# Kernel optimization log

Hardware: AMD Instinct MI355X
Metric: run time of the kernel (lower is better)

The kernel has to match this reference:

```python
import jax, jax.numpy as jnp
import numpy as np

SIZE = (128, 160, 128)  # (D, H, W)
BATCH, CHANNELS = 4, 1


def setup_inputs() -> dict:
    key = jax.random.key(0)
    k1, k2 = jax.random.split(key)
    src = jax.random.normal(k1, (BATCH, CHANNELS) + SIZE, dtype=jnp.float32)
    # near-identity affine [B, 3, 4] so most sampled coords land in-volume
    eye = jnp.concatenate([jnp.eye(3, dtype=jnp.float32), jnp.zeros((3, 1), jnp.float32)], axis=1)
    affine_matrix = eye[None] + 0.05 * jax.random.normal(k2, (BATCH, 3, 4), dtype=jnp.float32)
    return {"src": src, "affine_matrix": affine_matrix}


def _mesh_matrix(D, H, W):
    # rows: dim0 (D), dim1 (H), dim2 (W), ones  -> [4, N]
    gz, gy, gx = jnp.meshgrid(jnp.arange(D), jnp.arange(H), jnp.arange(W), indexing='ij')
    N = D * H * W
    return jnp.stack([gz.reshape(N), gy.reshape(N), gx.reshape(N),
                      jnp.ones((N,), jnp.int32)], axis=0).astype(jnp.float32)


def _trilinear_border(src, ix, iy, iz):
    # src: [B, C, D, H, W]; ix/iy/iz: [B, N] unnormalized pixel coords (x->W, y->H, z->D)
    B, C, D, H, W = src.shape
    # border padding: clamp coordinate before interpolation (matches PyTorch)
    ix = jnp.clip(ix, 0.0, W - 1.0)
    iy = jnp.clip(iy, 0.0, H - 1.0)
    iz = jnp.clip(iz, 0.0, D - 1.0)
    x0f, y0f, z0f = jnp.floor(ix), jnp.floor(iy), jnp.floor(iz)
    wx = (ix - x0f)[:, None, :]  # [B,1,N]
    wy = (iy - y0f)[:, None, :]
    wz = (iz - z0f)[:, None, :]
    x0 = x0f.astype(jnp.int32); x1 = jnp.minimum(x0 + 1, W - 1)
    y0 = y0f.astype(jnp.int32); y1 = jnp.minimum(y0 + 1, H - 1)
    z0 = z0f.astype(jnp.int32); z1 = jnp.minimum(z0 + 1, D - 1)
    flat = src.reshape(B, C, D * H * W)
    N = ix.shape[-1]

    def gather(zz, yy, xx):
        idx = (zz * H + yy) * W + xx  # [B, N]
        idx = jnp.broadcast_to(idx[:, None, :], (B, C, N))
        return jnp.take_along_axis(flat, idx, axis=2)  # [B, C, N]

    c000 = gather(z0, y0, x0); c001 = gather(z0, y0, x1)
    c010 = gather(z0, y1, x0); c011 = gather(z0, y1, x1)
    c100 = gather(z1, y0, x0); c101 = gather(z1, y0, x1)
    c110 = gather(z1, y1, x0); c111 = gather(z1, y1, x1)
    c00 = c000 + (c001 - c000) * wx
    c01 = c010 + (c011 - c010) * wx
    c10 = c100 + (c101 - c100) * wx
    c11 = c110 + (c111 - c110) * wx
    c0 = c00 + (c01 - c00) * wy
    c1 = c10 + (c11 - c10) * wy
    return c0 + (c1 - c0) * wz  # [B, C, N]


def reference(src, affine_matrix):
    D, H, W = SIZE
    B, C = src.shape[:2]
    mesh = _mesh_matrix(D, H, W)  # [4, N]
    loc = jnp.einsum('bij,jn->bin', affine_matrix, mesh)  # [B, 3, N] voxel coords
    sizes = jnp.array([D, H, W], jnp.float32)
    g = 2.0 * (loc / (sizes[None, :, None] - 1.0) - 0.5)  # normalized, dims (d0,d1,d2)
    # flip to grid_sample (x, y, z) ordering, then unnormalize (align_corners=False)
    ix = ((g[:, 2] + 1.0) * W - 1.0) * 0.5
    iy = ((g[:, 1] + 1.0) * H - 1.0) * 0.5
    iz = ((g[:, 0] + 1.0) * D - 1.0) * 0.5
    out = _trilinear_border(src, ix, iy, iz)  # [B, C, N]
    return out.reshape(B, C, D, H, W)
```

## Files before the change

kernel.cpp:

```cpp
#include <hip/hip_runtime.h>

#define DD 128
#define HH 160
#define WW 128
#define BB 4
#define HW  20480
#define DHW 2621440

#define TX 32
#define TY 8
#define TZ 8
#define XT 4
#define YT 20
#define ZT 16
#define NWG (XT * YT * ZT * BB)
#define NXCD 8
#define CPX (NWG / NXCD)

#define FZE   14
#define FYE   14
#define PITCH 44
#define CPRCH 11
#define SLABF (FYE * PITCH)
#define ROWB  (PITCH * 4)
#define SLABB (SLABF * 4)
#define SLABCH (FYE * CPRCH)
#define LDSALLOC 9216

typedef float f2 __attribute__((ext_vector_type(2), aligned(4)));
typedef float v2 __attribute__((ext_vector_type(2)));

__global__ __launch_bounds__(256)
void st_affine_kernel(const float* __restrict__ src,
                      const float* __restrict__ aff,
                      float* __restrict__ out) {
    __shared__ float lds[LDSALLOC];

    const int wgid = blockIdx.x;
    const int lin  = (wgid & (NXCD - 1)) * CPX + (wgid >> 3);
    const int xt = lin & 3;
    const int l2 = lin >> 2;
    const int yt = l2 % YT;
    const int l3 = l2 / YT;
    const int zt = l3 & (ZT - 1);
    const int b  = l3 >> 4;
    const int x0t = xt * TX, y0t = yt * TY, z0t = zt * TZ;

    const float* A = aff + b * 12;
    const float cD = 128.f/127.f, cH = 160.f/159.f, cW = 128.f/127.f;
    const float pz0 = A[0]*cD, pz1 = A[1]*cD, pz2 = A[2]*cD,  pz3 = fmaf(A[3],  cD, -0.5f);
    const float py0 = A[4]*cH, py1 = A[5]*cH, py2 = A[6]*cH,  py3 = fmaf(A[7],  cH, -0.5f);
    const float px0 = A[8]*cW, px1 = A[9]*cW, px2 = A[10]*cW, px3 = fmaf(A[11], cW, -0.5f);

    const float hz = (TZ - 1) * 0.5f, hy = (TY - 1) * 0.5f, hx = (TX - 1) * 0.5f;
    const float ccz = (float)z0t + hz, ccy = (float)y0t + hy, ccx = (float)x0t + hx;
    const float izcn = fmaf(pz0, ccz, fmaf(pz1, ccy, fmaf(pz2, ccx, pz3)));
    const float iycn = fmaf(py0, ccz, fmaf(py1, ccy, fmaf(py2, ccx, py3)));
    const float ixcn = fmaf(px0, ccz, fmaf(px1, ccy, fmaf(px2, ccx, px3)));
    const float rz = fmaf(fabsf(pz0), hz, fmaf(fabsf(pz1), hy, fmaf(fabsf(pz2), hx, 1e-3f)));
    const float ry = fmaf(fabsf(py0), hz, fmaf(fabsf(py1), hy, fmaf(fabsf(py2), hx, 1e-3f)));
    const float rx = fmaf(fabsf(px0), hz, fmaf(fabsf(px1), hy, fmaf(fabsf(px2), hx, 1e-3f)));
    const float mnz = izcn - rz, mxz = izcn + rz;
    const float mny = iycn - ry, mxy = iycn + ry;
    const float mnx = ixcn - rx, mxx = ixcn + rx;

    const bool interior =
        (mnz > 0.02f) && (mxz < 126.98f) &&
        (mny > 0.02f) && (mxy < 158.98f) &&
        (mnx > 0.02f) && (mxx < 126.98f);

    const int xlo = max(0, (int)floorf(__builtin_amdgcn_fmed3f(mnx, 0.f, 127.f)) - 1);
    const int ylo = max(0, (int)floorf(__builtin_amdgcn_fmed3f(mny, 0.f, 159.f)) - 1);
    const int zlo = max(0, (int)floorf(__builtin_amdgcn_fmed3f(mnz, 0.f, 127.f)) - 1);
    const int xhi = min(WW - 2, (int)floorf(__builtin_amdgcn_fmed3f(mxx, 0.f, 127.f)) + 1);
    const int yhi = min(HH - 2, (int)floorf(__builtin_amdgcn_fmed3f(mxy, 0.f, 159.f)) + 1);
    const int zhi = min(DD - 2, (int)floorf(__builtin_amdgcn_fmed3f(mxz, 0.f, 127.f)) + 1);

    const int xlo4 = xlo & ~3;
    const int XE4  = xhi - xlo4 + 2;
    const int YE   = yhi - ylo + 2;
    const int ZE   = zhi - zlo + 2;
    const bool fits = (XE4 <= PITCH) && (YE <= FYE) && (ZE <= FZE);

    const int tid  = threadIdx.x;
    const int lane = tid & 63;
    const int wid  = tid >> 6;

    const float zloF = (float)zlo, yloF = (float)ylo, xlo4F = (float)xlo4;

    const int xp = x0t + ((lane & 15) << 1);
    const int yo = y0t + (lane >> 4) + ((wid & 1) << 2);
    const int zb = z0t + ((wid >> 1) << 2);
    const float fx0 = (float)xp, fy = (float)yo, fzb = (float)zb;

    const float izb0 = fmaf(pz0, fzb, fmaf(pz1, fy, fmaf(pz2, fx0, pz3)));
    const float iyb0 = fmaf(py0, fzb, fmaf(py1, fy, fmaf(py2, fx0, py3)));
    const float ixb0 = fmaf(px0, fzb, fmaf(px1, fy, fmaf(px2, fx0, px3)));

    const float* sb = src + b * DHW;
    float* dst0 = out + (size_t)(((b * DD + zb) * HH + yo) * WW + xp);

    if (fits) {
        const float RC154 = 1.f / 154.f, RC11 = 1.f / 11.f;
        const float gbase = fmaf(zloF, 20480.f, fmaf(yloF, 128.f, xlo4F));
        const int totalCh = ZE * SLABCH;
        const int nIt = (totalCh + 255) >> 8;
        for (int it = 0; it < nIt; ++it) {
            const int k = (it << 8) + tid;
            float kf  = (float)k;
            float zif = floorf(fmaf(kf, RC154, 0.5f * RC154));
            float rem = fmaf(zif, -154.f, kf);
            float yif = floorf(fmaf(rem, RC11, 0.5f * RC11));
            float xif = fmaf(yif, -11.f, rem);
            float gf  = fmaf(zif, 20480.f, fmaf(yif, 128.f, fmaf(xif, 4.f, gbase)));
            int g = min((int)gf, DHW - 4);
            __builtin_amdgcn_global_load_lds(
                (const __attribute__((address_space(1))) void*)(sb + g),
                (__attribute__((address_space(3))) void*)(lds + (size_t)(((it << 8) + (wid << 6)) * 4)),
                16, 0, 0);
        }
    }
    __syncthreads();

    const char* Lb = (const char*)lds;

    auto triL = [&](int o0, int o1, v2 wx, v2 wy, v2 wz) -> v2 {
        f2 a00 = *(const f2*)(Lb + o0);
        f2 a01 = *(const f2*)(Lb + o0 + ROWB);
        f2 a10 = *(const f2*)(Lb + o0 + SLABB);
        f2 a11 = *(const f2*)(Lb + o0 + SLABB + ROWB);
        f2 b00 = *(const f2*)(Lb + o1);
        f2 b01 = *(const f2*)(Lb + o1 + ROWB);
        f2 b10 = *(const f2*)(Lb + o1 + SLABB);
        f2 b11 = *(const f2*)(Lb + o1 + SLABB + ROWB);
        v2 c00 = {fmaf(a00.y - a00.x, wx.x, a00.x), fmaf(b00.y - b00.x, wx.y, b00.x)};
        v2 c01 = {fmaf(a01.y - a01.x, wx.x, a01.x), fmaf(b01.y - b01.x, wx.y, b01.x)};
        v2 c10 = {fmaf(a10.y - a10.x, wx.x, a10.x), fmaf(b10.y - b10.x, wx.y, b10.x)};
        v2 c11 = {fmaf(a11.y - a11.x, wx.x, a11.x), fmaf(b11.y - b11.x, wx.y, b11.x)};
        v2 c0 = c00 + (c01 - c00) * wy;
        v2 c1 = c10 + (c11 - c10) * wy;
        return c0 + (c1 - c0) * wz;
    };

    if (fits) {
        const v2 dzv = {pz0, pz0}, dyv = {py0, py0}, dxv = {px0, px0};
        if (interior) {
            v2 az = {izb0 - zloF, izb0 + pz2 - zloF};
            v2 ay = {iyb0 - yloF, iyb0 + py2 - yloF};
            v2 ax = {ixb0 - xlo4F, ixb0 + px2 - xlo4F};
#pragma unroll
            for (int s = 0; s < 4; ++s) {
                v2 cz = {floorf(az.x), floorf(az.y)};
                v2 cy = {floorf(ay.x), floorf(ay.y)};
                v2 cx = {floorf(ax.x), floorf(ax.y)};
                v2 wz = az - cz, wy = ay - cy, wx = ax - cx;
                v2 ob = (cz * (float)FYE + cy) * (float)ROWB + cx * 4.f;
                v2 r = triL((int)ob.x, (int)ob.y, wx, wy, wz);
                __builtin_nontemporal_store(r, (v2*)(dst0 + s * HW));
                az += dzv; ay += dyv; ax += dxv;
            }
        } else {
            const float hiZ = 127.f - zloF, capZ = 126.f - zloF;
            const float hiY = 159.f - yloF, capY = 158.f - yloF;
            const float hiX = 127.f - xlo4F, capX = 126.f - xlo4F;
            v2 az = {izb0 - zloF, izb0 + pz2 - zloF};
            v2 ay = {iyb0 - yloF, iyb0 + py2 - yloF};
            v2 ax = {ixb0 - xlo4F, ixb0 + px2 - xlo4F};
#pragma unroll
            for (int s = 0; s < 4; ++s) {
                v2 azc = {__builtin_amdgcn_fmed3f(az.x, 0.f, hiZ),
                          __builtin_amdgcn_fmed3f(az.y, 0.f, hiZ)};
                v2 ayc = {__builtin_amdgcn_fmed3f(ay.x, 0.f, hiY),
                          __builtin_amdgcn_fmed3f(ay.y, 0.f, hiY)};
                v2 axc = {__builtin_amdgcn_fmed3f(ax.x, 0.f, hiX),
                          __builtin_amdgcn_fmed3f(ax.y, 0.f, hiX)};
                v2 cz = {fminf(floorf(azc.x), capZ), fminf(floorf(azc.y), capZ)};
                v2 cy = {fminf(floorf(ayc.x), capY), fminf(floorf(ayc.y), capY)};
                v2 cx = {fminf(floorf(axc.x), capX), fminf(floorf(axc.y), capX)};
                v2 wz = azc - cz, wy = ayc - cy, wx = axc - cx;
                v2 ob = (cz * (float)FYE + cy) * (float)ROWB + cx * 4.f;
                v2 r = triL((int)ob.x, (int)ob.y, wx, wy, wz);
                __builtin_nontemporal_store(r, (v2*)(dst0 + s * HW));
                az += dzv; ay += dyv; ax += dxv;
            }
        }
    } else {
        v2 az = {izb0, izb0 + pz2};
        v2 ay = {iyb0, iyb0 + py2};
        v2 ax = {ixb0, ixb0 + px2};
        const v2 dzv = {pz0, pz0}, dyv = {py0, py0}, dxv = {px0, px0};
#pragma unroll
        for (int s = 0; s < 4; ++s) {
            v2 azc = {__builtin_amdgcn_fmed3f(az.x, 0.f, 127.f),
                      __builtin_amdgcn_fmed3f(az.y, 0.f, 127.f)};
            v2 ayc = {__builtin_amdgcn_fmed3f(ay.x, 0.f, 159.f),
                      __builtin_amdgcn_fmed3f(ay.y, 0.f, 159.f)};
            v2 axc = {__builtin_amdgcn_fmed3f(ax.x, 0.f, 127.f),
                      __builtin_amdgcn_fmed3f(ax.y, 0.f, 127.f)};
            v2 cz = {fminf(floorf(azc.x), 126.f), fminf(floorf(azc.y), 126.f)};
            v2 cy = {fminf(floorf(ayc.x), 158.f), fminf(floorf(ayc.y), 158.f)};
            v2 cx = {fminf(floorf(axc.x), 126.f), fminf(floorf(axc.y), 126.f)};
            v2 wz = azc - cz, wy = ayc - cy, wx = axc - cx;
            auto g1 = [&](float czs, float cys, float cxs, float wxs, float wys, float wzs) -> float {
                int o = (int)fmaf(czs, 20480.f, fmaf(cys, 128.f, cxs));
                const float* p = sb + o;
                f2 v00 = *(const f2*)(p);
                f2 v01 = *(const f2*)(p + WW);
                f2 v10 = *(const f2*)(p + HW);
                f2 v11 = *(const f2*)(p + HW + WW);
                float c00 = fmaf(v00.y - v00.x, wxs, v00.x);
                float c01 = fmaf(v01.y - v01.x, wxs, v01.x);
                float c10 = fmaf(v10.y - v10.x, wxs, v10.x);
                float c11 = fmaf(v11.y - v11.x, wxs, v11.x);
                float c0 = fmaf(c01 - c00, wys, c00);
                float c1 = fmaf(c11 - c10, wys, c10);
                return fmaf(c1 - c0, wzs, c0);
            };
            v2 r;
            r.x = g1(cz.x, cy.x, cx.x, wx.x, wy.x, wz.x);
            r.y = g1(cz.y, cy.y, cx.y, wx.y, wy.y, wz.y);
            __builtin_nontemporal_store(r, (v2*)(dst0 + s * HW));
            az += dzv; ay += dyv; ax += dxv;
        }
    }
}

extern "C" void kernel_launch(void* const* d_in, const int* in_sizes, int n_in,
                              void* d_out, int out_size, void* d_ws, size_t ws_size,
                              hipStream_t stream) {
    const float* src = (const float*)d_in[0];
    const float* aff = (const float*)d_in[1];
    float* out = (float*)d_out;

    st_affine_kernel<<<dim3(NWG), dim3(256), 0, stream>>>(src, aff, out);
}
```

Measured before the change: 24.56 us.

## Split LDS halo wait so first z-slices compute while remaining loads land

The block's LDS fill now always issues a fixed, unrolled 9 iterations of global_load_lds. The single __syncthreads is replaced by a partial vmcnt wait plus barrier, which lets the first half of the output z-slices compute before the last loads finish when a bound check shows those slices only touch the early slabs. Work is remapped so each wave handles z offsets {0,1,4,5} instead of four consecutive slices, so the early pair depends only on low slabs. This risks correctness if the fixed iteration count or the vmcnt bookkeeping doesn't match the issued loads, and it adds redundant loads for small footprints.

Measured after the change: 25.89 us. 1.05x slower.

```diff
diff --git a/kernel.cpp b/kernel.cpp
--- a/kernel.cpp
+++ b/kernel.cpp
@@ -20,12 +20,12 @@
 #define FZE   14
 #define FYE   14
 #define PITCH 44
-#define CPRCH 11
 #define SLABF (FYE * PITCH)
 #define ROWB  (PITCH * 4)
 #define SLABB (SLABF * 4)
-#define SLABCH (FYE * CPRCH)
-#define LDSALLOC 9216
+#define SLABCH (FYE * 11)
+#define NIT 9
+#define LDSALLOC (NIT * 1024)
 
 typedef float f2 __attribute__((ext_vector_type(2), aligned(4)));
 typedef float v2 __attribute__((ext_vector_type(2)));
@@ -82,15 +82,21 @@
     const int ZE   = zhi - zlo + 2;
     const bool fits = (XE4 <= PITCH) && (YE <= FYE) && (ZE <= FZE);
 
+    const float zloF = (float)zlo, yloF = (float)ylo, xlo4F = (float)xlo4;
+
+    const float izs1max = fmaf(pz0, (float)z0t + 1.5f,
+                               fmaf(pz1, ccy, fmaf(pz2, ccx, pz3)))
+                        + fmaf(fabsf(pz0), 1.5f,
+                               fmaf(fabsf(pz1), hy, fmaf(fabsf(pz2), hx, 1e-3f)));
+    const bool splitOK = fits && (izs1max < zloF + 7.5f);
+
     const int tid  = threadIdx.x;
     const int lane = tid & 63;
     const int wid  = tid >> 6;
 
-    const float zloF = (float)zlo, yloF = (float)ylo, xlo4F = (float)xlo4;
-
     const int xp = x0t + ((lane & 15) << 1);
     const int yo = y0t + (lane >> 4) + ((wid & 1) << 2);
-    const int zb = z0t + ((wid >> 1) << 2);
+    const int zb = z0t + ((wid >> 1) << 1);
     const float fx0 = (float)xp, fy = (float)yo, fzb = (float)zb;
 
     const float izb0 = fmaf(pz0, fzb, fmaf(pz1, fy, fmaf(pz2, fx0, pz3)));
@@ -103,9 +109,8 @@
     if (fits) {
         const float RC154 = 1.f / 154.f, RC11 = 1.f / 11.f;
         const float gbase = fmaf(zloF, 20480.f, fmaf(yloF, 128.f, xlo4F));
-        const int totalCh = ZE * SLABCH;
-        const int nIt = (totalCh + 255) >> 8;
-        for (int it = 0; it < nIt; ++it) {
+#pragma unroll
+        for (int it = 0; it < NIT; ++it) {
             const int k = (it << 8) + tid;
             float kf  = (float)k;
             float zif = floorf(fmaf(kf, RC154, 0.5f * RC154));
@@ -120,7 +125,6 @@
                 16, 0, 0);
         }
     }
-    __syncthreads();
 
     const char* Lb = (const char*)lds;
 
@@ -144,51 +148,65 @@
 
     if (fits) {
         const v2 dzv = {pz0, pz0}, dyv = {py0, py0}, dxv = {px0, px0};
-        if (interior) {
-            v2 az = {izb0 - zloF, izb0 + pz2 - zloF};
-            v2 ay = {iyb0 - yloF, iyb0 + py2 - yloF};
-            v2 ax = {ixb0 - xlo4F, ixb0 + px2 - xlo4F};
-#pragma unroll
-            for (int s = 0; s < 4; ++s) {
-                v2 cz = {floorf(az.x), floorf(az.y)};
-                v2 cy = {floorf(ay.x), floorf(ay.y)};
-                v2 cx = {floorf(ax.x), floorf(ax.y)};
-                v2 wz = az - cz, wy = ay - cy, wx = ax - cx;
-                v2 ob = (cz * (float)FYE + cy) * (float)ROWB + cx * 4.f;
-                v2 r = triL((int)ob.x, (int)ob.y, wx, wy, wz);
-                __builtin_nontemporal_store(r, (v2*)(dst0 + s * HW));
-                az += dzv; ay += dyv; ax += dxv;
-            }
-        } else {
-            const float hiZ = 127.f - zloF, capZ = 126.f - zloF;
-            const float hiY = 159.f - yloF, capY = 158.f - yloF;
-            const float hiX = 127.f - xlo4F, capX = 126.f - xlo4F;
-            v2 az = {izb0 - zloF, izb0 + pz2 - zloF};
-            v2 ay = {iyb0 - yloF, iyb0 + py2 - yloF};
-            v2 ax = {ixb0 - xlo4F, ixb0 + px2 - xlo4F};
-#pragma unroll
-            for (int s = 0; s < 4; ++s) {
+        const float hiZ = 127.f - zloF, capZ = 126.f - zloF;
+        const float hiY = 159.f - yloF, capY = 158.f - yloF;
+        const float hiX = 127.f - xlo4F, capX = 126.f - xlo4F;
+
+        v2 az = {izb0 - zloF, izb0 + pz2 - zloF};
+        v2 ay = {iyb0 - yloF, iyb0 + py2 - yloF};
+        v2 ax = {ixb0 - xlo4F, ixb0 + px2 - xlo4F};
+
+        auto doPair = [&](float* d) {
+            v2 cz, cy, cx, wz, wy, wx;
+            if (interior) {
+                cz = v2{floorf(az.x), floorf(az.y)};
+                cy = v2{floorf(ay.x), floorf(ay.y)};
+                cx = v2{floorf(ax.x), floorf(ax.y)};
+                wz = az - cz; wy = ay - cy; wx = ax - cx;
+            } else {
                 v2 azc = {__builtin_amdgcn_fmed3f(az.x, 0.f, hiZ),
                           __builtin_amdgcn_fmed3f(az.y, 0.f, hiZ)};
                 v2 ayc = {__builtin_amdgcn_fmed3f(ay.x, 0.f, hiY),
                           __builtin_amdgcn_fmed3f(ay.y, 0.f, hiY)};
                 v2 axc = {__builtin_amdgcn_fmed3f(ax.x, 0.f, hiX),
                           __builtin_amdgcn_fmed3f(ax.y, 0.f, hiX)};
-                v2 cz = {fminf(floorf(azc.x), capZ), fminf(floorf(azc.y), capZ)};
-                v2 cy = {fminf(floorf(ayc.x), capY), fminf(floorf(ayc.y), capY)};
-                v2 cx = {fminf(floorf(axc.x), capX), fminf(floorf(axc.y), capX)};
-                v2 wz = azc - cz, wy = ayc - cy, wx = axc - cx;
-                v2 ob = (cz * (float)FYE + cy) * (float)ROWB + cx * 4.f;
-                v2 r = triL((int)ob.x, (int)ob.y, wx, wy, wz);
-                __builtin_nontemporal_store(r, (v2*)(dst0 + s * HW));
-                az += dzv; ay += dyv; ax += dxv;
+                cz = v2{fminf(floorf(azc.x), capZ), fminf(floorf(azc.y), capZ)};
+                cy = v2{fminf(floorf(ayc.x), capY), fminf(floorf(ayc.y), capY)};
+                cx = v2{fminf(floorf(axc.x), capX), fminf(floorf(axc.y), capX)};
+                wz = azc - cz; wy = ayc - cy; wx = axc - cx;
             }
+            v2 ob = (cz * (float)FYE + cy) * (float)ROWB + cx * 4.f;
+            v2 r = triL((int)ob.x, (int)ob.y, wx, wy, wz);
+            __builtin_nontemporal_store(r, (v2*)d);
+        };
+        auto adv = [&]() { az += dzv; ay += dyv; ax += dxv; };
+
+        if (splitOK) {
+            asm volatile("s_waitcnt vmcnt(3)" ::: "memory");
+        } else {
+            asm volatile("s_waitcnt vmcnt(0)" ::: "memory");
         }
+        __builtin_amdgcn_s_barrier();
+        __builtin_amdgcn_sched_barrier(0);
+
+        doPair(dst0);
+        adv();
+        doPair(dst0 + HW);
+
+        asm volatile("s_waitcnt vmcnt(2)" ::: "memory");
+        __builtin_amdgcn_s_barrier();
+        __builtin_amdgcn_sched_barrier(0);
+
+        adv(); adv(); adv();
+        doPair(dst0 + 4 * HW);
+        adv();
+        doPair(dst0 + 5 * HW);
     } else {
         v2 az = {izb0, izb0 + pz2};
         v2 ay = {iyb0, iyb0 + py2};
         v2 ax = {ixb0, ixb0 + px2};
         const v2 dzv = {pz0, pz0}, dyv = {py0, py0}, dxv = {px0, px0};
+        const int zoffs[4] = {0, 1, 4, 5};
 #pragma unroll
         for (int s = 0; s < 4; ++s) {
             v2 azc = {__builtin_amdgcn_fmed3f(az.x, 0.f, 127.f),
@@ -219,7 +237,9 @@
             v2 r;
             r.x = g1(cz.x, cy.x, cx.x, wx.x, wy.x, wz.x);
             r.y = g1(cz.y, cy.y, cx.y, wx.y, wy.y, wz.y);
-            __builtin_nontemporal_store(r, (v2*)(dst0 + s * HW));
+            __builtin_nontemporal_store(r, (v2*)(dst0 + zoffs[s] * HW));
+            if (s == 1) { az += dzv; ay += dyv; ax += dxv;
+                          az += dzv; ay += dyv; ax += dxv; }
             az += dzv; ay += dyv; ax += dxv;
         }
     }
```
